# Performance work log

Measured on AMD Instinct MI355X. Metric: run time of the kernel, lower is better.

The kernel has to match this reference:

```python
import jax, jax.numpy as jnp
import numpy as np

B, L = 4, 2048
D_MODEL = 64          # d_model = input_size
ED = 128              # d_inner = expand_factor * d_model = hidden_size
N = 32                # d_state
DCONV = 16            # d_conv
NLAYERS = 4
DTRANK = 4            # ceil(d_model/16)
NCLS = 1
EPS = 1e-5


def setup_inputs() -> dict:
    key = jax.random.key(0)
    ks = jax.random.split(key, 10)
    g = lambda k, s, sc: jax.random.normal(k, s, dtype=jnp.float32) * sc
    inp = {}
    inp["x"] = jax.random.normal(ks[0], (B, L, D_MODEL), dtype=jnp.float32)
    inp["in_w"] = g(ks[1], (NLAYERS, 2 * ED, D_MODEL), 0.1)
    inp["in_b"] = jnp.zeros((NLAYERS, 2 * ED), jnp.float32)
    inp["conv_w"] = g(ks[2], (NLAYERS, ED, 1, DCONV), 0.1)  # depthwise kernel (OIH per group)
    inp["conv_b"] = jnp.zeros((NLAYERS, ED), jnp.float32)
    inp["xproj_w"] = g(ks[3], (NLAYERS, DTRANK + 2 * N, ED), 0.1)
    inp["dtproj_w"] = g(ks[4], (NLAYERS, ED, DTRANK), 0.5)
    inp["dtproj_b"] = g(ks[5], (NLAYERS, ED), 0.5)
    # S4D-real init: A[e, n] = n+1
    A = jnp.tile(jnp.arange(1, N + 1, dtype=jnp.float32), (ED, 1))
    inp["A_log"] = jnp.tile(jnp.log(A)[None], (NLAYERS, 1, 1))
    inp["Dp"] = jnp.ones((NLAYERS, ED), jnp.float32)
    inp["outproj_w"] = g(ks[6], (NLAYERS, D_MODEL, ED), 0.1)
    inp["outproj_b"] = jnp.zeros((NLAYERS, D_MODEL), jnp.float32)
    inp["norm_w"] = jnp.ones((NLAYERS, D_MODEL), jnp.float32)
    inp["fc_w"] = g(ks[7], (NCLS, ED), 0.1)
    inp["fc_b"] = jnp.zeros((NCLS,), jnp.float32)
    return inp


def _rmsnorm(x, w):
    return x * jax.lax.rsqrt(jnp.mean(x * x, axis=-1, keepdims=True) + EPS) * w


def _causal_dwconv(x, w, b):
    # x: [B,L,ED], w: [ED,1,DCONV] depthwise, causal left pad
    xt = jnp.swapaxes(x, 1, 2)  # [B,ED,L]
    y = jax.lax.conv_general_dilated(
        xt, w, window_strides=(1,), padding=[(DCONV - 1, 0)],
        dimension_numbers=("NCH", "OIH", "NCH"), feature_group_count=ED)
    return jnp.swapaxes(y, 1, 2) + b


def _mamba_block(h, in_w, in_b, conv_w, conv_b, xproj_w, dtproj_w, dtproj_b,
                 A_log, Dp, outproj_w, outproj_b, last):
    xz = jnp.einsum("bld,ed->ble", h, in_w) + in_b          # [B,L,2ED]
    xin, z = jnp.split(xz, 2, axis=-1)
    xc = jax.nn.silu(_causal_dwconv(xin, conv_w, conv_b))    # [B,L,ED]
    dbc = jnp.einsum("ble,re->blr", xc, xproj_w)             # [B,L,DTRANK+2N]
    delta = dbc[..., :DTRANK]
    Bm = dbc[..., DTRANK:DTRANK + N]                          # [B,L,N]
    Cm = dbc[..., DTRANK + N:]                                # [B,L,N]
    delta = jax.nn.softplus(jnp.einsum("blr,er->ble", delta, dtproj_w) + dtproj_b)
    A = -jnp.exp(A_log)                                       # [ED,N]
    dA = jnp.exp(delta[..., None] * A)                        # [B,L,ED,N]
    dBu = delta[..., None] * Bm[:, :, None, :] * xc[..., None]  # [B,L,ED,N]

    def step(hs, t):
        dA_t, dBu_t, C_t = t                                  # [B,ED,N],[B,ED,N],[B,N]
        hs = dA_t * hs + dBu_t
        y = jnp.einsum("ben,bn->be", hs, C_t)
        return hs, y

    h0 = jnp.zeros((xc.shape[0], ED, N), dtype=xc.dtype)
    _, ys = jax.lax.scan(step, h0, (jnp.swapaxes(dA, 0, 1),
                                    jnp.swapaxes(dBu, 0, 1),
                                    jnp.swapaxes(Cm, 0, 1)))
    y = jnp.swapaxes(ys, 0, 1) + Dp * xc                      # [B,L,ED]
    y = y * jax.nn.silu(z)
    if last:
        return y                                              # classifier taps d_inner features
    return jnp.einsum("ble,de->bld", y, outproj_w) + outproj_b


def reference(x, in_w, in_b, conv_w, conv_b, xproj_w, dtproj_w, dtproj_b,
              A_log, Dp, outproj_w, outproj_b, norm_w, fc_w, fc_b):
    h = x
    for i in range(NLAYERS - 1):
        h = h + _mamba_block(_rmsnorm(h, norm_w[i]), in_w[i], in_b[i], conv_w[i],
                             conv_b[i], xproj_w[i], dtproj_w[i], dtproj_b[i],
                             A_log[i], Dp[i], outproj_w[i], outproj_b[i], False)
    i = NLAYERS - 1
    y = _mamba_block(_rmsnorm(h, norm_w[i]), in_w[i], in_b[i], conv_w[i],
                     conv_b[i], xproj_w[i], dtproj_w[i], dtproj_b[i],
                     A_log[i], Dp[i], outproj_w[i], outproj_b[i], True)
    last_hidden = y[:, -1, :]                                 # [B,ED]
    return last_hidden @ fc_w.T + fc_b                        # [B,NCLS]
```

## Files before the change

kernel.cpp:

```cpp
#include <hip/hip_runtime.h>
#include <math.h>

#define BSZ 4
#define Lseq 2048
#define DM 64
#define ED 128
#define NST 32
#define DCONVK 16
#define NLAYERS 4
#define DTRANK 4
#define EPSV 1e-5f
#define NC 128
#define TT 16

__device__ __forceinline__ float sigf(float x) { return 1.0f / (1.0f + __expf(-x)); }
__device__ __forceinline__ float hsum4(float4 a) { return (a.x + a.y) + (a.z + a.w); }

__device__ __forceinline__ void inproj16(
    const float* in_w_l, const float* in_b_l, const float (*hn)[DM],
    float* xin, float* zbuf, size_t t0, int tid)
{
    float4 w4[16];
    const float4* wr = (const float4*)(in_w_l + tid * DM);
    #pragma unroll
    for (int i = 0; i < 16; ++i) w4[i] = wr[i];
    const float bias = in_b_l[tid];
    #pragma unroll 2
    for (int tok = 0; tok < TT; ++tok) {
        const float4* hv4 = (const float4*)&hn[tok][0];
        float4 a4 = make_float4(0.f, 0.f, 0.f, 0.f);
        #pragma unroll
        for (int i = 0; i < 16; ++i) {
            float4 hv = hv4[i];
            a4.x = fmaf(hv.x, w4[i].x, a4.x);
            a4.y = fmaf(hv.y, w4[i].y, a4.y);
            a4.z = fmaf(hv.z, w4[i].z, a4.z);
            a4.w = fmaf(hv.w, w4[i].w, a4.w);
        }
        const float r = bias + hsum4(a4);
        if (tid < ED) xin[(t0 + tok) * ED + tid] = r;
        else          zbuf[(t0 + tok) * ED + (tid - ED)] = r;
    }
}

__global__ __launch_bounds__(256) void k_layer_gemm(
    const float* __restrict__ hin, const float* __restrict__ norm_w,
    const float* __restrict__ in_w, const float* __restrict__ in_b,
    float* __restrict__ xin, float* __restrict__ zb, float* __restrict__ out)
{
    const int t0 = blockIdx.x * TT;
    const int tid = threadIdx.x;
    const int lane = tid & 63;
    const int wv = tid >> 6;
    __shared__ __align__(16) float hn[TT][DM];

    if (blockIdx.x == 0 && tid < BSZ) out[tid] = 0.f;

    const float nw = norm_w[lane];
    float hval[4];
    #pragma unroll
    for (int j = 0; j < 4; ++j)
        hval[j] = hin[(size_t)(t0 + wv * 4 + j) * DM + lane];

    #pragma unroll
    for (int j = 0; j < 4; ++j) {
        float ss = hval[j] * hval[j];
        #pragma unroll
        for (int off = 32; off; off >>= 1) ss += __shfl_xor(ss, off, 64);
        const float sc = rsqrtf(ss * (1.0f / DM) + EPSV);
        hn[wv * 4 + j][lane] = hval[j] * sc * nw;
    }
    __syncthreads();
    inproj16(in_w, in_b, (const float (*)[DM])hn, xin, zb, (size_t)t0, tid);
}

__global__ __launch_bounds__(256) void k_conv_scan(
    const float* __restrict__ xin, const float* __restrict__ conv_w,
    const float* __restrict__ conv_b, const float* __restrict__ xproj_w,
    const float* __restrict__ dtproj_w, const float* __restrict__ dtproj_b,
    const float* __restrict__ A_log,
    float* __restrict__ xc_out, float* __restrict__ delta_out,
    float* __restrict__ Bout, float* __restrict__ Cout,
    float* __restrict__ aprod, float* __restrict__ hloc, int store_dbc)
{
    const int blk = blockIdx.x;
    const int b   = blk >> 7;
    const int c   = blk & 127;
    const int l0  = c * TT;
    const size_t t0 = (size_t)b * Lseq + l0;
    const int tid = threadIdx.x;
    const int e = tid & 127, half = tid >> 7;
    const bool doXC = store_dbc || (c == NC - 1);
    __shared__ __align__(16) float xs[(TT + DCONVK - 1) * ED];
    __shared__ __align__(16) float xcs[TT][ED];
    __shared__ __align__(16) float Bs[TT][NST];
    __shared__ float dts[TT][DTRANK];
    float (*dl)[ED] = (float (*)[ED])xs;

    float Aen16[16];
    {
        const float4* a4 = (const float4*)(A_log + e * NST + half * 16);
        #pragma unroll
        for (int i = 0; i < 4; ++i) {
            float4 v = a4[i];
            Aen16[i*4+0] = -__expf(v.x); Aen16[i*4+1] = -__expf(v.y);
            Aen16[i*4+2] = -__expf(v.z); Aen16[i*4+3] = -__expf(v.w);
        }
    }
    float w[DCONVK];
    {
        const float4* cw = (const float4*)(conv_w + e * DCONVK);
        #pragma unroll
        for (int i = 0; i < 4; ++i) {
            float4 cc = cw[i];
            w[i*4+0] = cc.x; w[i*4+1] = cc.y; w[i*4+2] = cc.z; w[i*4+3] = cc.w;
        }
    }
    const float cb = conv_b[e];

    {
        const int NV = (TT + DCONVK - 1) * ED / 4;
        for (int idx4 = tid; idx4 < NV; idx4 += 256) {
            const int row = idx4 >> 5;
            const int lrow = l0 - (DCONVK - 1) + row;
            float4 v = make_float4(0.f, 0.f, 0.f, 0.f);
            if (lrow >= 0)
                v = ((const float4*)(xin + ((size_t)b * Lseq + lrow) * ED))[idx4 & 31];
            ((float4*)xs)[idx4] = v;
        }
    }
    __syncthreads();

    {
        #pragma unroll 2
        for (int j = 0; j < 8; ++j) {
            const int tok = half * 8 + j;
            float acc = cb;
            #pragma unroll
            for (int k = 0; k < DCONVK; ++k)
                acc = fmaf(xs[(tok + k) * ED + e], w[k], acc);
            const float xcv = acc * sigf(acc);
            xcs[tok][e] = xcv;
            if (doXC) xc_out[(t0 + tok) * ED + e] = xcv;
        }
    }
    __syncthreads();

    {
        const int wv = tid >> 6, lane = tid & 63;
        float4 acc[4];
        #pragma unroll
        for (int j = 0; j < 4; ++j) acc[j] = make_float4(0.f, 0.f, 0.f, 0.f);
        #pragma unroll 1
        for (int p = 0; p < 4; ++p) {
            float4 w4[8];
            const float4* wr = (const float4*)(xproj_w + lane * ED + p * 32);
            #pragma unroll
            for (int i = 0; i < 8; ++i) w4[i] = wr[i];
            #pragma unroll
            for (int j = 0; j < 4; ++j) {
                const float4* yv = (const float4*)&xcs[wv * 4 + j][p * 32];
                #pragma unroll
                for (int i = 0; i < 8; ++i) {
                    float4 hv = yv[i];
                    acc[j].x = fmaf(hv.x, w4[i].x, acc[j].x);
                    acc[j].y = fmaf(hv.y, w4[i].y, acc[j].y);
                    acc[j].z = fmaf(hv.z, w4[i].z, acc[j].z);
                    acc[j].w = fmaf(hv.w, w4[i].w, acc[j].w);
                }
            }
        }
        #pragma unroll
        for (int j = 0; j < 4; ++j) {
            const int tok = wv * 4 + j;
            const float v = hsum4(acc[j]);
            if (lane < DTRANK) {
                dts[tok][lane] = v;
            } else if (lane < DTRANK + NST) {
                Bs[tok][lane - DTRANK] = v;
                if (store_dbc) Bout[(t0 + tok) * NST + (lane - DTRANK)] = v;
            } else {
                if (doXC) Cout[(t0 + tok) * NST + (lane - DTRANK - NST)] = v;
            }
        }
        {
            const int ridx = lane & 3;
            const int ks   = (lane >> 2) & 3;
            const int tsub = lane >> 4;
            const int r4   = 64 + ridx;
            const int tok  = wv * 4 + tsub;
            const float4* wr = (const float4*)(xproj_w + r4 * ED + ks * 32);
            const float4* yv = (const float4*)&xcs[tok][ks * 32];
            float4 a4 = make_float4(0.f, 0.f, 0.f, 0.f);
            #pragma unroll
            for (int i = 0; i < 8; ++i) {
                float4 hv = yv[i]; float4 wv4 = wr[i];
                a4.x = fmaf(hv.x, wv4.x, a4.x);
                a4.y = fmaf(hv.y, wv4.y, a4.y);
                a4.z = fmaf(hv.z, wv4.z, a4.z);
                a4.w = fmaf(hv.w, wv4.w, a4.w);
            }
            float v = hsum4(a4);
            v += __shfl_xor(v, 4, 64);
            v += __shfl_xor(v, 8, 64);
            if (ks == 0 && doXC) Cout[(t0 + tok) * NST + (r4 - DTRANK - NST)] = v;
        }
    }
    __syncthreads();

    {
        const float4 dwv = *(const float4*)(dtproj_w + e * DTRANK);
        const float bias = dtproj_b[e];
        #pragma unroll 2
        for (int j = 0; j < 8; ++j) {
            const int tok = half * 8 + j;
            float a = bias;
            a = fmaf(dts[tok][0], dwv.x, a);
            a = fmaf(dts[tok][1], dwv.y, a);
            a = fmaf(dts[tok][2], dwv.z, a);
            a = fmaf(dts[tok][3], dwv.w, a);
            const float sp = fmaxf(a, 0.f) + log1pf(__expf(-fabsf(a)));
            dl[tok][e] = sp;
            if (store_dbc) delta_out[(t0 + tok) * ED + e] = sp;
        }
    }
    __syncthreads();

    {
        float dsum = 0.f;
        #pragma unroll 4
        for (int l = 0; l < TT; ++l) dsum += dl[l][e];

        #pragma unroll 1
        for (int g = 0; g < 2; ++g) {
            const int n0 = half * 16 + g * 8;
            float Aen[8];
            #pragma unroll
            for (int k = 0; k < 8; ++k) Aen[k] = Aen16[g * 8 + k];
            float hs[8];
            #pragma unroll
            for (int k = 0; k < 8; ++k) hs[k] = 0.f;
            #pragma unroll 2
            for (int l = 0; l < TT; ++l) {
                const float de   = dl[l][e];
                const float dexc = de * xcs[l][e];
                const float4 B0 = *(const float4*)&Bs[l][n0];
                const float4 B1 = *(const float4*)&Bs[l][n0 + 4];
                float a;
                a = __expf(de * Aen[0]); hs[0] = fmaf(a, hs[0], B0.x * dexc);
                a = __expf(de * Aen[1]); hs[1] = fmaf(a, hs[1], B0.y * dexc);
                a = __expf(de * Aen[2]); hs[2] = fmaf(a, hs[2], B0.z * dexc);
                a = __expf(de * Aen[3]); hs[3] = fmaf(a, hs[3], B0.w * dexc);
                a = __expf(de * Aen[4]); hs[4] = fmaf(a, hs[4], B1.x * dexc);
                a = __expf(de * Aen[5]); hs[5] = fmaf(a, hs[5], B1.y * dexc);
                a = __expf(de * Aen[6]); hs[6] = fmaf(a, hs[6], B1.z * dexc);
                a = __expf(de * Aen[7]); hs[7] = fmaf(a, hs[7], B1.w * dexc);
            }
            const size_t idx = (((size_t)b * NC + c) * ED + e) * NST + n0;
            *(float4*)(hloc + idx)     = make_float4(hs[0], hs[1], hs[2], hs[3]);
            *(float4*)(hloc + idx + 4) = make_float4(hs[4], hs[5], hs[6], hs[7]);
            *(float4*)(aprod + idx) =
                make_float4(__expf(Aen[0] * dsum), __expf(Aen[1] * dsum),
                            __expf(Aen[2] * dsum), __expf(Aen[3] * dsum));
            *(float4*)(aprod + idx + 4) =
                make_float4(__expf(Aen[4] * dsum), __expf(Aen[5] * dsum),
                            __expf(Aen[6] * dsum), __expf(Aen[7] * dsum));
        }
    }
}

__global__ __launch_bounds__(64) void k_scan_combine(
    const float* __restrict__ aprod, float* __restrict__ hloc,
    const float* __restrict__ Cv, const float* __restrict__ xc,
    const float* __restrict__ zb, const float* __restrict__ Dp,
    const float* __restrict__ fcw, const float* __restrict__ fcb,
    float* __restrict__ out, int final)
{
    const int t = blockIdx.x * 64 + threadIdx.x;
    const int b = t >> 12;
    const int en = t & 4095;
    size_t idx = (size_t)b * NC * (ED * NST) + en;
    float h = 0.f;
    #pragma unroll 4
    for (int c = 0; c < NC; ++c) {
        const float a = aprod[idx];
        const float u = hloc[idx];
        hloc[idx] = h;
        h = fmaf(a, h, u);
        idx += ED * NST;
    }
    if (final) {
        const int e = en >> 5, n = en & 31;
        const size_t tok = (size_t)b * Lseq + (Lseq - 1);
        float p = h * Cv[tok * NST + n];
        #pragma unroll
        for (int off = 16; off; off >>= 1) p += __shfl_xor(p, off, 32);
        if (n == 0) {
            const float xce = xc[tok * ED + e];
            const float zi  = zb[tok * ED + e];
            float val = (p + Dp[e] * xce) * (zi * sigf(zi)) * fcw[e];
            if (en == 0) val += fcb[0];
            atomicAdd(&out[b], val);
        }
    }
}

__global__ __launch_bounds__(256) void k_scan_gemm(
    const float* __restrict__ delta, const float* __restrict__ Bv,
    const float* __restrict__ Cv, const float* __restrict__ xc,
    const float* __restrict__ zbin, const float* __restrict__ A_log,
    const float* __restrict__ Dp, const float* __restrict__ hinit,
    const float* __restrict__ ow, const float* __restrict__ ob,
    const float* __restrict__ hin, const float* __restrict__ norm_w,
    const float* __restrict__ in_w, const float* __restrict__ in_b,
    float* __restrict__ hout, float* __restrict__ xin, float* __restrict__ zb)
{
    const int blk = blockIdx.x;
    const int b   = blk >> 7;
    const int c   = blk & 127;
    const int l0  = c * TT;
    const size_t t0 = (size_t)b * Lseq + l0;
    const int tid = threadIdx.x;
    const int e = tid & 127, half = tid >> 7;

    __shared__ __align__(16) float dlS[TT][ED];
    __shared__ __align__(16) float xcS[TT][ED];
    __shared__ __align__(16) float BsS[TT][NST];
    __shared__ __align__(16) float CsS[TT][NST];
    __shared__ __align__(16) float ys[TT][ED];
    __shared__ __align__(16) float pp[2][TT][ED];
    __shared__ __align__(16) float hn[TT][DM];

    float Aen16[16];
    {
        const float4* a4 = (const float4*)(A_log + e * NST + half * 16);
        #pragma unroll
        for (int i = 0; i < 4; ++i) {
            float4 v = a4[i];
            Aen16[i*4+0] = -__expf(v.x); Aen16[i*4+1] = -__expf(v.y);
            Aen16[i*4+2] = -__expf(v.z); Aen16[i*4+3] = -__expf(v.w);
        }
    }

    {
        const float4* dsrc = (const float4*)(delta + t0 * ED);
        const float4* xsrc = (const float4*)(xc + t0 * ED);
        float4* ddst = (float4*)&dlS[0][0];
        float4* xdst = (float4*)&xcS[0][0];
        #pragma unroll
        for (int i = 0; i < 2; ++i) {
            ddst[tid + i * 256] = dsrc[tid + i * 256];
            xdst[tid + i * 256] = xsrc[tid + i * 256];
        }
        if (tid < 128) {
            ((float4*)&BsS[0][0])[tid] = ((const float4*)(Bv + t0 * NST))[tid];
            ((float4*)&CsS[0][0])[tid] = ((const float4*)(Cv + t0 * NST))[tid];
        }
    }
    __syncthreads();

    #pragma unroll 1
    for (int g = 0; g < 2; ++g) {
        const int n0 = half * 16 + g * 8;
        float Aen[8];
        #pragma unroll
        for (int k = 0; k < 8; ++k) Aen[k] = Aen16[g * 8 + k];
        float hs[8];
        {
            const size_t idx = (((size_t)b * NC + c) * ED + e) * NST + n0;
            const float4 h0 = *(const float4*)(hinit + idx);
            const float4 h1 = *(const float4*)(hinit + idx + 4);
            hs[0] = h0.x; hs[1] = h0.y; hs[2] = h0.z; hs[3] = h0.w;
            hs[4] = h1.x; hs[5] = h1.y; hs[6] = h1.z; hs[7] = h1.w;
        }
        #pragma unroll 2
        for (int l = 0; l < TT; ++l) {
            const float de   = dlS[l][e];
            const float dexc = de * xcS[l][e];
            const float4 B0 = *(const float4*)&BsS[l][n0];
            const float4 B1 = *(const float4*)&BsS[l][n0 + 4];
            const float4 C0 = *(const float4*)&CsS[l][n0];
            const float4 C1 = *(const float4*)&CsS[l][n0 + 4];
            float a, p = 0.f;
            a = __expf(de * Aen[0]); hs[0] = fmaf(a, hs[0], B0.x * dexc); p = fmaf(hs[0], C0.x, p);
            a = __expf(de * Aen[1]); hs[1] = fmaf(a, hs[1], B0.y * dexc); p = fmaf(hs[1], C0.y, p);
            a = __expf(de * Aen[2]); hs[2] = fmaf(a, hs[2], B0.z * dexc); p = fmaf(hs[2], C0.z, p);
            a = __expf(de * Aen[3]); hs[3] = fmaf(a, hs[3], B0.w * dexc); p = fmaf(hs[3], C0.w, p);
            a = __expf(de * Aen[4]); hs[4] = fmaf(a, hs[4], B1.x * dexc); p = fmaf(hs[4], C1.x, p);
            a = __expf(de * Aen[5]); hs[5] = fmaf(a, hs[5], B1.y * dexc); p = fmaf(hs[5], C1.y, p);
            a = __expf(de * Aen[6]); hs[6] = fmaf(a, hs[6], B1.z * dexc); p = fmaf(hs[6], C1.z, p);
            a = __expf(de * Aen[7]); hs[7] = fmaf(a, hs[7], B1.w * dexc); p = fmaf(hs[7], C1.w, p);
            if (g == 0) pp[half][l][e] = p;
            else        pp[half][l][e] += p;
        }
    }
    __syncthreads();
    {
        const float dpe = Dp[e];
        #pragma unroll 2
        for (int j = 0; j < 8; ++j) {
            const int tl = half * 8 + j;
            const size_t tok = t0 + tl;
            const float p = pp[0][tl][e] + pp[1][tl][e];
            const float zi = zbin[tok * ED + e];
            ys[tl][e] = (p + dpe * xcS[tl][e]) * (zi * sigf(zi));
        }
    }
    __syncthreads();

    const int lane = tid & 63;
    const int wv = tid >> 6;
    const float nw = norm_w[lane];
    float hval[4];
    {
        float4 acc[4];
        #pragma unroll
        for (int j = 0; j < 4; ++j) acc[j] = make_float4(0.f, 0.f, 0.f, 0.f);
        #pragma unroll 1
        for (int p = 0; p < 4; ++p) {
            float4 w4[8];
            const float4* wr = (const float4*)(ow + lane * ED + p * 32);
            #pragma unroll
            for (int q = 0; q < 8; ++q) w4[q] = wr[q];
            #pragma unroll
            for (int j = 0; j < 4; ++j) {
                const float4* yv = (const float4*)&ys[wv * 4 + j][p * 32];
                #pragma unroll
                for (int q = 0; q < 8; ++q) {
                    float4 hv = yv[q];
                    acc[j].x = fmaf(hv.x, w4[q].x, acc[j].x);
                    acc[j].y = fmaf(hv.y, w4[q].y, acc[j].y);
                    acc[j].z = fmaf(hv.z, w4[q].z, acc[j].z);
                    acc[j].w = fmaf(hv.w, w4[q].w, acc[j].w);
                }
            }
        }
        const float obd = ob[lane];
        #pragma unroll
        for (int j = 0; j < 4; ++j) {
            const size_t tok = t0 + wv * 4 + j;
            hval[j] = hsum4(acc[j]) + obd + hin[tok * DM + lane];
            hout[tok * DM + lane] = hval[j];
        }
    }
    #pragma unroll
    for (int j = 0; j < 4; ++j) {
        float ss = hval[j] * hval[j];
        #pragma unroll
        for (int off = 32; off; off >>= 1) ss += __shfl_xor(ss, off, 64);
        const float sc = rsqrtf(ss * (1.0f / DM) + EPSV);
        hn[wv * 4 + j][lane] = hval[j] * sc * nw;
    }
    __syncthreads();
    inproj16(in_w, in_b, (const float (*)[DM])hn, xin, zb, t0, tid);
}

extern "C" void kernel_launch(void* const* d_in, const int* in_sizes, int n_in,
                              void* d_out, int out_size, void* d_ws, size_t ws_size,
                              hipStream_t stream)
{
    const float* x         = (const float*)d_in[0];
    const float* in_w      = (const float*)d_in[1];
    const float* in_b      = (const float*)d_in[2];
    const float* conv_w    = (const float*)d_in[3];
    const float* conv_b    = (const float*)d_in[4];
    const float* xproj_w   = (const float*)d_in[5];
    const float* dtproj_w  = (const float*)d_in[6];
    const float* dtproj_b  = (const float*)d_in[7];
    const float* A_log     = (const float*)d_in[8];
    const float* Dp        = (const float*)d_in[9];
    const float* outproj_w = (const float*)d_in[10];
    const float* outproj_b = (const float*)d_in[11];
    const float* norm_w    = (const float*)d_in[12];
    const float* fc_w      = (const float*)d_in[13];
    const float* fc_b      = (const float*)d_in[14];

    const size_t TOK = (size_t)BSZ * Lseq;
    float* ws = (float*)d_ws;
    float* h0    = ws; ws += TOK * DM;
    float* h1    = ws; ws += TOK * DM;
    float* xin   = ws; ws += TOK * ED;
    float* zbuf  = ws; ws += TOK * ED;
    float* xc    = ws; ws += TOK * ED;
    float* dlt   = ws; ws += TOK * ED;
    float* Bv    = ws; ws += TOK * NST;
    float* Cv    = ws; ws += TOK * NST;
    float* aprod = ws; ws += (size_t)BSZ * NC * ED * NST;
    float* hloc  = ws; ws += (size_t)BSZ * NC * ED * NST;

    const float* hres = x;
    float* hbufs[2] = { h0, h1 };

    k_layer_gemm<<<(int)(TOK / TT), 256, 0, stream>>>(
        x, norm_w, in_w, in_b, xin, zbuf, (float*)d_out);

    for (int i = 0; i < NLAYERS; ++i) {
        const int last = (i == NLAYERS - 1);
        const float* Alog_i = A_log + (size_t)i * ED * NST;
        k_conv_scan<<<(int)(BSZ * NC), 256, 0, stream>>>(
            xin, conv_w + (size_t)i * ED * DCONVK, conv_b + (size_t)i * ED,
            xproj_w + (size_t)i * (DTRANK + 2 * NST) * ED,
            dtproj_w + (size_t)i * ED * DTRANK, dtproj_b + (size_t)i * ED,
            Alog_i, xc, dlt, Bv, Cv, aprod, hloc, last ? 0 : 1);
        k_scan_combine<<<(BSZ * ED * NST) / 64, 64, 0, stream>>>(
            aprod, hloc, Cv, xc, zbuf, Dp + (size_t)i * ED,
            fc_w, fc_b, (float*)d_out, last ? 1 : 0);
        if (!last) {
            float* hout = hbufs[i & 1];
            k_scan_gemm<<<(int)(BSZ * NC), 256, 0, stream>>>(
                dlt, Bv, Cv, xc, zbuf, Alog_i, Dp + (size_t)i * ED, hloc,
                outproj_w + (size_t)i * DM * ED, outproj_b + (size_t)i * DM,
                hres, norm_w + (size_t)(i + 1) * DM,
                in_w + (size_t)(i + 1) * 2 * ED * DM,
                in_b + (size_t)(i + 1) * 2 * ED,
                hout, xin, zbuf);
            hres = hout;
        }
    }
}
```

Measured before the change: 377.6 us.

## Recompute chunk decay from dsum and split scan combine into parallel segments

```diff
diff --git a/kernel.cpp b/kernel.cpp
--- a/kernel.cpp
+++ b/kernel.cpp
@@ -12,6 +12,18 @@
 #define EPSV 1e-5f
 #define NC 128
 #define TT 16
+#define NSEG 8
+#define L2E 1.4426950408889634f
+
+#if defined(__has_builtin)
+#if __has_builtin(__builtin_amdgcn_exp2f)
+#define EXP2F(x) __builtin_amdgcn_exp2f(x)
+#else
+#define EXP2F(x) exp2f(x)
+#endif
+#else
+#define EXP2F(x) exp2f(x)
+#endif
 
 __device__ __forceinline__ float sigf(float x) { return 1.0f / (1.0f + __expf(-x)); }
 __device__ __forceinline__ float hsum4(float4 a) { return (a.x + a.y) + (a.z + a.w); }
@@ -81,7 +93,7 @@
     const float* __restrict__ A_log,
     float* __restrict__ xc_out, float* __restrict__ delta_out,
     float* __restrict__ Bout, float* __restrict__ Cout,
-    float* __restrict__ aprod, float* __restrict__ hloc, int store_dbc)
+    float* __restrict__ dsum_out, float* __restrict__ hloc, int store_dbc)
 {
     const int blk = blockIdx.x;
     const int b   = blk >> 7;
@@ -103,8 +115,8 @@
         #pragma unroll
         for (int i = 0; i < 4; ++i) {
             float4 v = a4[i];
-            Aen16[i*4+0] = -__expf(v.x); Aen16[i*4+1] = -__expf(v.y);
-            Aen16[i*4+2] = -__expf(v.z); Aen16[i*4+3] = -__expf(v.w);
+            Aen16[i*4+0] = -__expf(v.x) * L2E; Aen16[i*4+1] = -__expf(v.y) * L2E;
+            Aen16[i*4+2] = -__expf(v.z) * L2E; Aen16[i*4+3] = -__expf(v.w) * L2E;
         }
     }
     float w[DCONVK];
@@ -230,6 +242,7 @@
         float dsum = 0.f;
         #pragma unroll 4
         for (int l = 0; l < TT; ++l) dsum += dl[l][e];
+        if (half == 0) dsum_out[((size_t)b * NC + c) * ED + e] = dsum;
 
         #pragma unroll 1
         for (int g = 0; g < 2; ++g) {
@@ -247,50 +260,73 @@
                 const float4 B0 = *(const float4*)&Bs[l][n0];
                 const float4 B1 = *(const float4*)&Bs[l][n0 + 4];
                 float a;
-                a = __expf(de * Aen[0]); hs[0] = fmaf(a, hs[0], B0.x * dexc);
-                a = __expf(de * Aen[1]); hs[1] = fmaf(a, hs[1], B0.y * dexc);
-                a = __expf(de * Aen[2]); hs[2] = fmaf(a, hs[2], B0.z * dexc);
-                a = __expf(de * Aen[3]); hs[3] = fmaf(a, hs[3], B0.w * dexc);
-                a = __expf(de * Aen[4]); hs[4] = fmaf(a, hs[4], B1.x * dexc);
-                a = __expf(de * Aen[5]); hs[5] = fmaf(a, hs[5], B1.y * dexc);
-                a = __expf(de * Aen[6]); hs[6] = fmaf(a, hs[6], B1.z * dexc);
-                a = __expf(de * Aen[7]); hs[7] = fmaf(a, hs[7], B1.w * dexc);
+                a = EXP2F(de * Aen[0]); hs[0] = fmaf(a, hs[0], B0.x * dexc);
+                a = EXP2F(de * Aen[1]); hs[1] = fmaf(a, hs[1], B0.y * dexc);
+                a = EXP2F(de * Aen[2]); hs[2] = fmaf(a, hs[2], B0.z * dexc);
+                a = EXP2F(de * Aen[3]); hs[3] = fmaf(a, hs[3], B0.w * dexc);
+                a = EXP2F(de * Aen[4]); hs[4] = fmaf(a, hs[4], B1.x * dexc);
+                a = EXP2F(de * Aen[5]); hs[5] = fmaf(a, hs[5], B1.y * dexc);
+                a = EXP2F(de * Aen[6]); hs[6] = fmaf(a, hs[6], B1.z * dexc);
+                a = EXP2F(de * Aen[7]); hs[7] = fmaf(a, hs[7], B1.w * dexc);
             }
             const size_t idx = (((size_t)b * NC + c) * ED + e) * NST + n0;
             *(float4*)(hloc + idx)     = make_float4(hs[0], hs[1], hs[2], hs[3]);
             *(float4*)(hloc + idx + 4) = make_float4(hs[4], hs[5], hs[6], hs[7]);
-            *(float4*)(aprod + idx) =
-                make_float4(__expf(Aen[0] * dsum), __expf(Aen[1] * dsum),
-                            __expf(Aen[2] * dsum), __expf(Aen[3] * dsum));
-            *(float4*)(aprod + idx + 4) =
-                make_float4(__expf(Aen[4] * dsum), __expf(Aen[5] * dsum),
-                            __expf(Aen[6] * dsum), __expf(Aen[7] * dsum));
         }
     }
 }
 
-__global__ __launch_bounds__(64) void k_scan_combine(
-    const float* __restrict__ aprod, float* __restrict__ hloc,
+__global__ __launch_bounds__(256) void k_scan_combine(
+    const float* __restrict__ dsum, float* __restrict__ hloc,
+    const float* __restrict__ A_log,
     const float* __restrict__ Cv, const float* __restrict__ xc,
     const float* __restrict__ zb, const float* __restrict__ Dp,
     const float* __restrict__ fcw, const float* __restrict__ fcb,
     float* __restrict__ out, int final)
 {
-    const int t = blockIdx.x * 64 + threadIdx.x;
-    const int b = t >> 12;
-    const int en = t & 4095;
-    size_t idx = (size_t)b * NC * (ED * NST) + en;
+    const int tid = threadIdx.x;
+    const int tt  = tid & 31;
+    const int seg = tid >> 5;
+    const int t   = blockIdx.x * 32 + tt;
+    const int b   = t >> 12;
+    const int en  = t & 4095;
+    const int e   = en >> 5;
+
+    const float Aen2 = -__expf(A_log[en]) * L2E;
+
+    const int c0 = seg * (NC / NSEG);
+    const size_t idxBase = (size_t)b * NC * (ED * NST) + en;
+    const size_t dBase   = (size_t)b * NC * ED + e;
+
+    float u[NC / NSEG], a[NC / NSEG];
+    #pragma unroll
+    for (int k = 0; k < NC / NSEG; ++k)
+        u[k] = hloc[idxBase + (size_t)(c0 + k) * (ED * NST)];
+    #pragma unroll
+    for (int k = 0; k < NC / NSEG; ++k)
+        a[k] = EXP2F(Aen2 * dsum[dBase + (size_t)(c0 + k) * ED]);
+
+    float A = 1.f, U = 0.f;
+    #pragma unroll
+    for (int k = 0; k < NC / NSEG; ++k) { U = fmaf(a[k], U, u[k]); A *= a[k]; }
+
+    __shared__ float As[NSEG][32], Us[NSEG][32];
+    As[seg][tt] = A; Us[seg][tt] = U;
+    __syncthreads();
+
     float h = 0.f;
-    #pragma unroll 4
-    for (int c = 0; c < NC; ++c) {
-        const float a = aprod[idx];
-        const float u = hloc[idx];
-        hloc[idx] = h;
-        h = fmaf(a, h, u);
-        idx += ED * NST;
-    }
-    if (final) {
-        const int e = en >> 5, n = en & 31;
+    #pragma unroll
+    for (int j = 0; j < NSEG - 1; ++j)
+        if (j < seg) h = fmaf(As[j][tt], h, Us[j][tt]);
+
+    #pragma unroll
+    for (int k = 0; k < NC / NSEG; ++k) {
+        hloc[idxBase + (size_t)(c0 + k) * (ED * NST)] = h;
+        h = fmaf(a[k], h, u[k]);
+    }
+
+    if (final && seg == NSEG - 1) {
+        const int n = en & 31;
         const size_t tok = (size_t)b * Lseq + (Lseq - 1);
         float p = h * Cv[tok * NST + n];
         #pragma unroll
@@ -337,8 +373,8 @@
         #pragma unroll
         for (int i = 0; i < 4; ++i) {
             float4 v = a4[i];
-            Aen16[i*4+0] = -__expf(v.x); Aen16[i*4+1] = -__expf(v.y);
-            Aen16[i*4+2] = -__expf(v.z); Aen16[i*4+3] = -__expf(v.w);
+            Aen16[i*4+0] = -__expf(v.x) * L2E; Aen16[i*4+1] = -__expf(v.y) * L2E;
+            Aen16[i*4+2] = -__expf(v.z) * L2E; Aen16[i*4+3] = -__expf(v.w) * L2E;
         }
     }
 
@@ -382,14 +418,14 @@
             const float4 C0 = *(const float4*)&CsS[l][n0];
             const float4 C1 = *(const float4*)&CsS[l][n0 + 4];
             float a, p = 0.f;
-            a = __expf(de * Aen[0]); hs[0] = fmaf(a, hs[0], B0.x * dexc); p = fmaf(hs[0], C0.x, p);
-            a = __expf(de * Aen[1]); hs[1] = fmaf(a, hs[1], B0.y * dexc); p = fmaf(hs[1], C0.y, p);
-            a = __expf(de * Aen[2]); hs[2] = fmaf(a, hs[2], B0.z * dexc); p = fmaf(hs[2], C0.z, p);
-            a = __expf(de * Aen[3]); hs[3] = fmaf(a, hs[3], B0.w * dexc); p = fmaf(hs[3], C0.w, p);
-            a = __expf(de * Aen[4]); hs[4] = fmaf(a, hs[4], B1.x * dexc); p = fmaf(hs[4], C1.x, p);
-            a = __expf(de * Aen[5]); hs[5] = fmaf(a, hs[5], B1.y * dexc); p = fmaf(hs[5], C1.y, p);
-            a = __expf(de * Aen[6]); hs[6] = fmaf(a, hs[6], B1.z * dexc); p = fmaf(hs[6], C1.z, p);
-            a = __expf(de * Aen[7]); hs[7] = fmaf(a, hs[7], B1.w * dexc); p = fmaf(hs[7], C1.w, p);
+            a = EXP2F(de * Aen[0]); hs[0] = fmaf(a, hs[0], B0.x * dexc); p = fmaf(hs[0], C0.x, p);
+            a = EXP2F(de * Aen[1]); hs[1] = fmaf(a, hs[1], B0.y * dexc); p = fmaf(hs[1], C0.y, p);
+            a = EXP2F(de * Aen[2]); hs[2] = fmaf(a, hs[2], B0.z * dexc); p = fmaf(hs[2], C0.z, p);
+            a = EXP2F(de * Aen[3]); hs[3] = fmaf(a, hs[3], B0.w * dexc); p = fmaf(hs[3], C0.w, p);
+            a = EXP2F(de * Aen[4]); hs[4] = fmaf(a, hs[4], B1.x * dexc); p = fmaf(hs[4], C1.x, p);
+            a = EXP2F(de * Aen[5]); hs[5] = fmaf(a, hs[5], B1.y * dexc); p = fmaf(hs[5], C1.y, p);
+            a = EXP2F(de * Aen[6]); hs[6] = fmaf(a, hs[6], B1.z * dexc); p = fmaf(hs[6], C1.z, p);
+            a = EXP2F(de * Aen[7]); hs[7] = fmaf(a, hs[7], B1.w * dexc); p = fmaf(hs[7], C1.w, p);
             if (g == 0) pp[half][l][e] = p;
             else        pp[half][l][e] += p;
         }
@@ -485,7 +521,7 @@
     float* dlt   = ws; ws += TOK * ED;
     float* Bv    = ws; ws += TOK * NST;
     float* Cv    = ws; ws += TOK * NST;
-    float* aprod = ws; ws += (size_t)BSZ * NC * ED * NST;
+    float* dsum  = ws; ws += (size_t)BSZ * NC * ED;
     float* hloc  = ws; ws += (size_t)BSZ * NC * ED * NST;
 
     const float* hres = x;
@@ -501,9 +537,9 @@
             xin, conv_w + (size_t)i * ED * DCONVK, conv_b + (size_t)i * ED,
             xproj_w + (size_t)i * (DTRANK + 2 * NST) * ED,
             dtproj_w + (size_t)i * ED * DTRANK, dtproj_b + (size_t)i * ED,
-            Alog_i, xc, dlt, Bv, Cv, aprod, hloc, last ? 0 : 1);
-        k_scan_combine<<<(BSZ * ED * NST) / 64, 64, 0, stream>>>(
-            aprod, hloc, Cv, xc, zbuf, Dp + (size_t)i * ED,
+            Alog_i, xc, dlt, Bv, Cv, dsum, hloc, last ? 0 : 1);
+        k_scan_combine<<<(BSZ * ED * NST * NSEG) / 256, 256, 0, stream>>>(
+            dsum, hloc, Alog_i, Cv, xc, zbuf, Dp + (size_t)i * ED,
             fc_w, fc_b, (float*)d_out, last ? 1 : 0);
         if (!last) {
             float* hout = hbufs[i & 1];
```

Measured after the change: 308.1 us. 1.23x faster.
